# Performance work log

Hardware: AMD Instinct MI355X
Metric: run time of the kernel (lower is better)

The kernel has to match this reference:

```python
import jax, jax.numpy as jnp
import numpy as np

B, S, D = 2, 2048, 1024
H = 16
DK = D // H  # attn_dim // num_heads = 64
DV = D // H  # embed_dim // num_heads = 64
NEG = -1e9


def setup_inputs() -> dict:
    key = jax.random.key(0)
    ks = jax.random.split(key, 6)
    inputs = jax.random.normal(ks[0], (B, S, D), dtype=jnp.float32)
    # mask[b, i, j]: key position i may attend to query position j when i <= j (causal)
    mask = jnp.broadcast_to(jnp.triu(jnp.ones((S, S), dtype=bool))[None], (B, S, S))
    sd = 1.0 / np.sqrt(D)
    WQ = jax.random.normal(ks[1], (D, H, DK), dtype=jnp.float32) * sd
    WK = jax.random.normal(ks[2], (D, H, DK), dtype=jnp.float32) * sd
    WV = jax.random.normal(ks[3], (D, H, DV), dtype=jnp.float32) * sd
    WO = jax.random.normal(ks[4], (D, D), dtype=jnp.float32) * sd
    bO = jnp.zeros((D,), dtype=jnp.float32)
    return {"inputs": inputs, "mask": mask, "WQ": WQ, "WK": WK, "WV": WV, "WO": WO, "bO": bO}


def reference(inputs, mask, WQ, WK, WV, WO, bO):
    scale = 1.0 / jnp.sqrt(jnp.float32(DK))
    q = jnp.einsum('bid,dhk->bihk', inputs, WQ) * scale
    k = jnp.einsum('bid,dhk->bihk', inputs, WK)
    v = jnp.einsum('bid,dhv->bihv', inputs, WV)
    # scores: [b, i, j, h]; softmax over axis=1 (key axis i), as in the original
    scores = jnp.einsum('bihd,bjhd->bijh', q, k)
    scores = jnp.where(mask[..., None], scores, NEG)
    attn = jax.nn.softmax(scores, axis=1)
    x = jnp.einsum('bijh,bihv->bjhv', attn, v)  # output indexed by query j
    x = x.reshape(B, S, D)
    return x @ WO + bO
```

## Files before the change

kernel.cpp:

```cpp
#include <hip/hip_runtime.h>
#include <hip/hip_bf16.h>


typedef __bf16 bf16;
typedef __bf16 bf16x8 __attribute__((ext_vector_type(8)));
typedef __bf16 bf16x4 __attribute__((ext_vector_type(4)));
typedef float  f32x4  __attribute__((ext_vector_type(4)));

constexpr int Sq = 2048;
constexpr int Dm = 1024;
constexpr int Hh = 16;

#define KSCALE 0.18033688011112042f

static __device__ __forceinline__ void gload_lds16(const bf16* g, bf16* l) {
  __builtin_amdgcn_global_load_lds(
      (const __attribute__((address_space(1))) unsigned int*)g,
      (__attribute__((address_space(3))) unsigned int*)l, 16, 0, 0);
}

__global__ __launch_bounds__(256) void cvt_bf16(
    const float* __restrict__ src, bf16* __restrict__ dst, int n) {
  const int i = (blockIdx.x * 256 + threadIdx.x) * 8;
  if (i >= n) return;
  float4 a = *reinterpret_cast<const float4*>(src + i);
  float4 b = *reinterpret_cast<const float4*>(src + i + 4);
  bf16x8 o;
  o[0] = (bf16)a.x; o[1] = (bf16)a.y; o[2] = (bf16)a.z; o[3] = (bf16)a.w;
  o[4] = (bf16)b.x; o[5] = (bf16)b.y; o[6] = (bf16)b.z; o[7] = (bf16)b.w;
  *reinterpret_cast<bf16x8*>(dst + i) = o;
}

__global__ __launch_bounds__(256) void tposeW4(
    const float* __restrict__ WQ, const float* __restrict__ WK,
    const float* __restrict__ WV, const float* __restrict__ WO,
    bf16* __restrict__ out) {
  __shared__ bf16 t[64][65];
  const int z = blockIdx.z;
  const float* in = (z == 0) ? WQ : (z == 1) ? WK : (z == 2) ? WV : WO;
  bf16* op = out + (size_t)z * 1024 * 1024;
  const int r0 = blockIdx.y * 64, c0 = blockIdx.x * 64;
  const int tid = threadIdx.x;
  const int rr = tid >> 3, cc = (tid & 7) * 8;
#pragma unroll
  for (int it = 0; it < 2; ++it) {
    int row = rr + it * 32;
    const float* ip = in + (size_t)(r0 + row) * 1024 + c0 + cc;
    float4 a = *reinterpret_cast<const float4*>(ip);
    float4 b = *reinterpret_cast<const float4*>(ip + 4);
    t[row][cc + 0] = (bf16)a.x; t[row][cc + 1] = (bf16)a.y;
    t[row][cc + 2] = (bf16)a.z; t[row][cc + 3] = (bf16)a.w;
    t[row][cc + 4] = (bf16)b.x; t[row][cc + 5] = (bf16)b.y;
    t[row][cc + 6] = (bf16)b.z; t[row][cc + 7] = (bf16)b.w;
  }
  __syncthreads();
#pragma unroll
  for (int it = 0; it < 2; ++it) {
    int crow = rr + it * 32;
    alignas(16) bf16 o[8];
#pragma unroll
    for (int e = 0; e < 8; ++e) o[e] = t[cc + e][crow];
    *reinterpret_cast<bf16x8*>(op + (size_t)(c0 + crow) * 1024 + r0 + cc) =
        *reinterpret_cast<bf16x8*>(o);
  }
}

template <int EPI, int MT>
__global__ __launch_bounds__(256) void gemm128(
    const bf16* __restrict__ A, const bf16* __restrict__ Bt,
    const int M, const int N, const int K,
    bf16* __restrict__ Katt, bf16* __restrict__ Qatt, bf16* __restrict__ VattT,
    const float* __restrict__ bOf, float* __restrict__ Cout) {
  constexpr int MF = MT / 32;
  __shared__ bf16 As[MT * 64], Bs[8192];
  const int tid = threadIdx.x;
  const int lane = tid & 63;
  const int w = tid >> 6;
  const int wr = w >> 1, wc = w & 1;
  const int g = lane >> 4, c = lane & 15;
  const int m0 = blockIdx.y * MT, n0 = blockIdx.x * 128;
  const int sr = lane >> 3;
  const int scp = ((lane & 7) ^ sr) * 8;

  f32x4 acc[MF][4];
#pragma unroll
  for (int i = 0; i < MF; ++i)
#pragma unroll
    for (int j = 0; j < 4; ++j) acc[i][j] = f32x4{0.f, 0.f, 0.f, 0.f};

  for (int k0 = 0; k0 < K; k0 += 64) {
#pragma unroll
    for (int p = 0; p < MT / 32; ++p) {
      const int rowb = p * 32 + w * 8;
      gload_lds16(A + (size_t)(m0 + rowb + sr) * K + k0 + scp, &As[rowb * 64]);
    }
#pragma unroll
    for (int p = 0; p < 4; ++p) {
      const int rowb = p * 32 + w * 8;
      gload_lds16(Bt + (size_t)(n0 + rowb + sr) * K + k0 + scp, &Bs[rowb * 64]);
    }
    __syncthreads();
#pragma unroll
    for (int kk = 0; kk < 2; ++kk) {
      const int ch = kk * 4 + g;
      bf16x8 af[MF], bfr[4];
#pragma unroll
      for (int mf = 0; mf < MF; ++mf) {
        const int row = wr * (MT / 2) + mf * 16 + c;
        af[mf] = *reinterpret_cast<const bf16x8*>(
            &As[row * 64 + ((ch ^ (row & 7)) << 3)]);
      }
#pragma unroll
      for (int nf = 0; nf < 4; ++nf) {
        const int row = wc * 64 + nf * 16 + c;
        bfr[nf] = *reinterpret_cast<const bf16x8*>(
            &Bs[row * 64 + ((ch ^ (row & 7)) << 3)]);
      }
#pragma unroll
      for (int mf = 0; mf < MF; ++mf)
#pragma unroll
        for (int nf = 0; nf < 4; ++nf)
          acc[mf][nf] = __builtin_amdgcn_mfma_f32_16x16x32_bf16(
              af[mf], bfr[nf], acc[mf][nf], 0, 0, 0);
    }
    __syncthreads();
  }

#pragma unroll
  for (int mf = 0; mf < MF; ++mf)
#pragma unroll
    for (int nf = 0; nf < 4; ++nf) {
      const int n = n0 + wc * 64 + nf * 16 + c;
      const int mb = m0 + wr * (MT / 2) + mf * 16 + g * 4;
      if (EPI == 0 && n >= 2048) {
        bf16x4 pk;
#pragma unroll
        for (int r = 0; r < 4; ++r) pk[r] = (bf16)acc[mf][nf][r];
        const int b = mb >> 11, sb = mb & (Sq - 1);
        const int h = (n >> 6) & 15, dk = n & 63;
        *reinterpret_cast<bf16x4*>(
            &VattT[((size_t)(b * Hh + h) * 64 + dk) * Sq + sb]) = pk;
      } else {
#pragma unroll
        for (int r = 0; r < 4; ++r) {
          const int m = mb + r;
          float v = acc[mf][nf][r];
          if (EPI == 0) {
            const int b = m >> 11, s = m & (Sq - 1);
            const int h = (n >> 6) & 15, dk = n & 63;
            const int bh = b * Hh + h;
            if (n < 1024)
              Katt[((size_t)bh * Sq + s) * 64 + dk] = (bf16)(v * KSCALE);
            else
              Qatt[((size_t)bh * Sq + s) * 64 + dk] = (bf16)v;
          } else {
            Cout[(size_t)m * N + n] = v + bOf[n];
          }
        }
      }
    }
}

__global__ __launch_bounds__(256, 4) void attn_v4(
    const bf16* __restrict__ Q, const bf16* __restrict__ K,
    const bf16* __restrict__ Vt, bf16* __restrict__ X) {
  __shared__ bf16 Kb[2][4096];
  __shared__ bf16 Vb[2][4096];
  __shared__ bf16 Pb[4096];
  const int tid = threadIdx.x, lane = tid & 63, w = tid >> 6;
  const int g = lane >> 4, c = lane & 15;
  const int bx = blockIdx.x;
  const int u = bx >> 5;
  const int bh = bx & 31;
  const int um = (u + 8 * (bh >> 3)) & 31;
  const int qblk = (um < 16) ? um : 47 - um;
  const int b = bh >> 4, h = bh & 15;
  const size_t base = (size_t)bh * Sq * 64;
  const bf16* Kg = K + base;
  const bf16* Vg = Vt + (size_t)bh * 64 * Sq;
  const int trow = tid >> 3, tch = tid & 7;
  bf16* Pw = Pb + w * 16 * 64;

  bf16x8 qf[2];
  {
    const bf16* Qg = Q + base + ((size_t)qblk * 64 + w * 16 + c) * 64;
    qf[0] = *reinterpret_cast<const bf16x8*>(Qg + g * 8);
    qf[1] = *reinterpret_cast<const bf16x8*>(Qg + 32 + g * 8);
  }

#pragma unroll
  for (int pp = 0; pp < 2; ++pp) {
    int row = trow + pp * 32;
    *reinterpret_cast<bf16x8*>(&Kb[0][row * 64 + ((tch ^ (row & 7)) << 3)]) =
        *reinterpret_cast<const bf16x8*>(Kg + (size_t)row * 64 + tch * 8);
    *reinterpret_cast<bf16x8*>(&Vb[0][row * 64 + ((tch ^ (row & 7)) << 3)]) =
        *reinterpret_cast<const bf16x8*>(Vg + (size_t)row * Sq + tch * 8);
  }
  __syncthreads();

  f32x4 acc[4];
  float lpart[4] = {0.f, 0.f, 0.f, 0.f};
#pragma unroll
  for (int vg = 0; vg < 4; ++vg) acc[vg] = f32x4{0.f, 0.f, 0.f, 0.f};

  const int ntiles = qblk + 1;
  for (int t = 0; t < ntiles; ++t) {
    const int cur = t & 1;
    const bf16* Kc = Kb[cur];
    const bf16* Vc = Vb[cur];
    const bool hasnext = (t + 1 < ntiles);

    bf16x8 kr0, kr1, vr0, vr1;
    if (hasnext) {
      const int i1 = (t + 1) * 64;
      kr0 = *reinterpret_cast<const bf16x8*>(Kg + (size_t)(i1 + trow) * 64 + tch * 8);
      kr1 = *reinterpret_cast<const bf16x8*>(Kg + (size_t)(i1 + trow + 32) * 64 + tch * 8);
      vr0 = *reinterpret_cast<const bf16x8*>(Vg + (size_t)trow * Sq + i1 + tch * 8);
      vr1 = *reinterpret_cast<const bf16x8*>(Vg + (size_t)(trow + 32) * Sq + i1 + tch * 8);
    }

    f32x4 sc[4];
#pragma unroll
    for (int kg = 0; kg < 4; ++kg) sc[kg] = f32x4{0.f, 0.f, 0.f, 0.f};
#pragma unroll
    for (int kk = 0; kk < 2; ++kk) {
      const int ch = kk * 4 + g;
#pragma unroll
      for (int kg = 0; kg < 4; ++kg) {
        int row = kg * 16 + c;
        bf16x8 kf = *reinterpret_cast<const bf16x8*>(
            &Kc[row * 64 + ((ch ^ (row & 7)) << 3)]);
        sc[kg] = __builtin_amdgcn_mfma_f32_16x16x32_bf16(qf[kk], kf, sc[kg], 0, 0, 0);
      }
    }

    const bool diag = (t == qblk);
#pragma unroll
    for (int kg = 0; kg < 4; ++kg)
#pragma unroll
      for (int r = 0; r < 4; ++r) {
        float p = __builtin_amdgcn_exp2f(sc[kg][r]);
        if (diag) {
          const int i = kg * 16 + c;
          const int j = w * 16 + g * 4 + r;
          p = (i <= j) ? p : 0.f;
        }
        lpart[r] += p;
        const int prow = g * 4 + r, pcol = kg * 16 + c;
        Pw[prow * 64 + (((pcol >> 3) ^ (prow & 7)) << 3) + (pcol & 7)] = (bf16)p;
      }

#pragma unroll
    for (int ks = 0; ks < 2; ++ks) {
      const int ch = ks * 4 + g;
      bf16x8 pf = *reinterpret_cast<const bf16x8*>(
          &Pw[c * 64 + ((ch ^ (c & 7)) << 3)]);
#pragma unroll
      for (int vg = 0; vg < 4; ++vg) {
        int dv = vg * 16 + c;
        bf16x8 vf = *reinterpret_cast<const bf16x8*>(
            &Vc[dv * 64 + ((ch ^ (dv & 7)) << 3)]);
        acc[vg] = __builtin_amdgcn_mfma_f32_16x16x32_bf16(pf, vf, acc[vg], 0, 0, 0);
      }
    }

    if (hasnext) {
      bf16* Kn = Kb[cur ^ 1];
      bf16* Vn = Vb[cur ^ 1];
      const int row0 = trow, row1 = trow + 32;
      *reinterpret_cast<bf16x8*>(&Kn[row0 * 64 + ((tch ^ (row0 & 7)) << 3)]) = kr0;
      *reinterpret_cast<bf16x8*>(&Kn[row1 * 64 + ((tch ^ (row1 & 7)) << 3)]) = kr1;
      *reinterpret_cast<bf16x8*>(&Vn[row0 * 64 + ((tch ^ (row0 & 7)) << 3)]) = vr0;
      *reinterpret_cast<bf16x8*>(&Vn[row1 * 64 + ((tch ^ (row1 & 7)) << 3)]) = vr1;
    }
    __syncthreads();
  }

  float linv[4];
#pragma unroll
  for (int r = 0; r < 4; ++r) {
    float l = lpart[r];
    l += __shfl_xor(l, 1);
    l += __shfl_xor(l, 2);
    l += __shfl_xor(l, 4);
    l += __shfl_xor(l, 8);
    linv[r] = 1.f / l;
  }
#pragma unroll
  for (int vg = 0; vg < 4; ++vg)
#pragma unroll
    for (int r = 0; r < 4; ++r) {
      const int j = qblk * 64 + w * 16 + g * 4 + r;
      const int dv = vg * 16 + c;
      X[((size_t)b * Sq + j) * Dm + h * 64 + dv] = (bf16)(acc[vg][r] * linv[r]);
    }
}

extern "C" void kernel_launch(void* const* d_in, const int* in_sizes, int n_in,
                              void* d_out, int out_size, void* d_ws, size_t ws_size,
                              hipStream_t stream) {
  const float* inputs = (const float*)d_in[0];
  const float* WQ = (const float*)d_in[2];
  const float* WK = (const float*)d_in[3];
  const float* WV = (const float*)d_in[4];
  const float* WO = (const float*)d_in[5];
  const float* bO = (const float*)d_in[6];
  float* out = (float*)d_out;

  bf16* Xin   = (bf16*)d_ws;
  bf16* Wt    = Xin + 4096 * 1024;
  bf16* Katt  = Wt + 4 * 1024 * 1024;
  bf16* Qatt  = Katt + (1 << 22);
  bf16* VattT = Qatt + (1 << 22);
  bf16* X     = Xin;

  cvt_bf16<<<2048, 256, 0, stream>>>(inputs, Xin, 4096 * 1024);

  tposeW4<<<dim3(16, 16, 4), 256, 0, stream>>>(WQ, WK, WV, WO, Wt);

  gemm128<0, 128><<<dim3(24, 32), 256, 0, stream>>>(
      Xin, Wt, 4096, 3072, 1024, Katt, Qatt, VattT, nullptr, nullptr);

  attn_v4<<<dim3(1024), 256, 0, stream>>>(Qatt, Katt, VattT, X);

  gemm128<1, 64><<<dim3(8, 64), 256, 0, stream>>>(
      X, Wt + 3 * 1024 * 1024, 4096, 1024, 1024,
      nullptr, nullptr, nullptr, bO, out);
}
```

Before: 108.2 us.

## Load K/V fragments directly from global in attention and merge prep kernels

The attention kernel drops the double-buffered LDS staging of K and V tiles along with the per-tile __syncthreads. Each wave now loads its MFMA operand fragments straight from global memory, relying on L2/L1 to serve the reuse across the four waves of a block. Separately, the bf16 input conversion and the weight transpose are merged into one launch to save a kernel launch. The risk is more global traffic and exposed load latency, since there is no longer an explicit prefetch of the next tile.

```diff
diff --git a/kernel.cpp b/kernel.cpp
--- a/kernel.cpp
+++ b/kernel.cpp
@@ -19,28 +19,30 @@
       (__attribute__((address_space(3))) unsigned int*)l, 16, 0, 0);
 }
 
-__global__ __launch_bounds__(256) void cvt_bf16(
-    const float* __restrict__ src, bf16* __restrict__ dst, int n) {
-  const int i = (blockIdx.x * 256 + threadIdx.x) * 8;
-  if (i >= n) return;
-  float4 a = *reinterpret_cast<const float4*>(src + i);
-  float4 b = *reinterpret_cast<const float4*>(src + i + 4);
-  bf16x8 o;
-  o[0] = (bf16)a.x; o[1] = (bf16)a.y; o[2] = (bf16)a.z; o[3] = (bf16)a.w;
-  o[4] = (bf16)b.x; o[5] = (bf16)b.y; o[6] = (bf16)b.z; o[7] = (bf16)b.w;
-  *reinterpret_cast<bf16x8*>(dst + i) = o;
-}
-
-__global__ __launch_bounds__(256) void tposeW4(
+__global__ __launch_bounds__(256) void prep(
+    const float* __restrict__ inputs,
     const float* __restrict__ WQ, const float* __restrict__ WK,
     const float* __restrict__ WV, const float* __restrict__ WO,
-    bf16* __restrict__ out) {
+    bf16* __restrict__ Xin, bf16* __restrict__ Wt) {
   __shared__ bf16 t[64][65];
-  const int z = blockIdx.z;
+  const int bx = blockIdx.x;
+  const int tid = threadIdx.x;
+  if (bx < 2048) {
+    const int i = (bx * 256 + tid) * 8;
+    float4 a = *reinterpret_cast<const float4*>(inputs + i);
+    float4 b = *reinterpret_cast<const float4*>(inputs + i + 4);
+    bf16x8 o;
+    o[0] = (bf16)a.x; o[1] = (bf16)a.y; o[2] = (bf16)a.z; o[3] = (bf16)a.w;
+    o[4] = (bf16)b.x; o[5] = (bf16)b.y; o[6] = (bf16)b.z; o[7] = (bf16)b.w;
+    *reinterpret_cast<bf16x8*>(Xin + i) = o;
+    return;
+  }
+  const int rr0 = bx - 2048;
+  const int z = rr0 >> 8;
+  const int tt = rr0 & 255;
+  const int r0 = (tt >> 4) * 64, c0 = (tt & 15) * 64;
   const float* in = (z == 0) ? WQ : (z == 1) ? WK : (z == 2) ? WV : WO;
-  bf16* op = out + (size_t)z * 1024 * 1024;
-  const int r0 = blockIdx.y * 64, c0 = blockIdx.x * 64;
-  const int tid = threadIdx.x;
+  bf16* op = Wt + (size_t)z * 1024 * 1024;
   const int rr = tid >> 3, cc = (tid & 7) * 8;
 #pragma unroll
   for (int it = 0; it < 2; ++it) {
@@ -161,11 +163,9 @@
     }
 }
 
-__global__ __launch_bounds__(256, 4) void attn_v4(
+__global__ __launch_bounds__(256, 4) void attn_v5(
     const bf16* __restrict__ Q, const bf16* __restrict__ K,
     const bf16* __restrict__ Vt, bf16* __restrict__ X) {
-  __shared__ bf16 Kb[2][4096];
-  __shared__ bf16 Vb[2][4096];
   __shared__ bf16 Pb[4096];
   const int tid = threadIdx.x, lane = tid & 63, w = tid >> 6;
   const int g = lane >> 4, c = lane & 15;
@@ -178,8 +178,7 @@
   const size_t base = (size_t)bh * Sq * 64;
   const bf16* Kg = K + base;
   const bf16* Vg = Vt + (size_t)bh * 64 * Sq;
-  const int trow = tid >> 3, tch = tid & 7;
-  bf16* Pw = Pb + w * 16 * 64;
+  bf16* Pw = Pb + w * 1024;
 
   bf16x8 qf[2];
   {
@@ -188,16 +187,6 @@
     qf[1] = *reinterpret_cast<const bf16x8*>(Qg + 32 + g * 8);
   }
 
-#pragma unroll
-  for (int pp = 0; pp < 2; ++pp) {
-    int row = trow + pp * 32;
-    *reinterpret_cast<bf16x8*>(&Kb[0][row * 64 + ((tch ^ (row & 7)) << 3)]) =
-        *reinterpret_cast<const bf16x8*>(Kg + (size_t)row * 64 + tch * 8);
-    *reinterpret_cast<bf16x8*>(&Vb[0][row * 64 + ((tch ^ (row & 7)) << 3)]) =
-        *reinterpret_cast<const bf16x8*>(Vg + (size_t)row * Sq + tch * 8);
-  }
-  __syncthreads();
-
   f32x4 acc[4];
   float lpart[4] = {0.f, 0.f, 0.f, 0.f};
 #pragma unroll
@@ -205,34 +194,32 @@
 
   const int ntiles = qblk + 1;
   for (int t = 0; t < ntiles; ++t) {
-    const int cur = t & 1;
-    const bf16* Kc = Kb[cur];
-    const bf16* Vc = Vb[cur];
-    const bool hasnext = (t + 1 < ntiles);
-
-    bf16x8 kr0, kr1, vr0, vr1;
-    if (hasnext) {
-      const int i1 = (t + 1) * 64;
-      kr0 = *reinterpret_cast<const bf16x8*>(Kg + (size_t)(i1 + trow) * 64 + tch * 8);
-      kr1 = *reinterpret_cast<const bf16x8*>(Kg + (size_t)(i1 + trow + 32) * 64 + tch * 8);
-      vr0 = *reinterpret_cast<const bf16x8*>(Vg + (size_t)trow * Sq + i1 + tch * 8);
-      vr1 = *reinterpret_cast<const bf16x8*>(Vg + (size_t)(trow + 32) * Sq + i1 + tch * 8);
-    }
+    const bf16* Kt = Kg + (size_t)t * 64 * 64;
+    bf16x8 kf[2][4];
+#pragma unroll
+    for (int kk = 0; kk < 2; ++kk)
+#pragma unroll
+      for (int kg = 0; kg < 4; ++kg)
+        kf[kk][kg] = *reinterpret_cast<const bf16x8*>(
+            Kt + (kg * 16 + c) * 64 + kk * 32 + g * 8);
 
     f32x4 sc[4];
 #pragma unroll
     for (int kg = 0; kg < 4; ++kg) sc[kg] = f32x4{0.f, 0.f, 0.f, 0.f};
 #pragma unroll
-    for (int kk = 0; kk < 2; ++kk) {
-      const int ch = kk * 4 + g;
-#pragma unroll
-      for (int kg = 0; kg < 4; ++kg) {
-        int row = kg * 16 + c;
-        bf16x8 kf = *reinterpret_cast<const bf16x8*>(
-            &Kc[row * 64 + ((ch ^ (row & 7)) << 3)]);
-        sc[kg] = __builtin_amdgcn_mfma_f32_16x16x32_bf16(qf[kk], kf, sc[kg], 0, 0, 0);
-      }
-    }
+    for (int kk = 0; kk < 2; ++kk)
+#pragma unroll
+      for (int kg = 0; kg < 4; ++kg)
+        sc[kg] = __builtin_amdgcn_mfma_f32_16x16x32_bf16(
+            qf[kk], kf[kk][kg], sc[kg], 0, 0, 0);
+
+    bf16x8 vf[2][4];
+#pragma unroll
+    for (int ks = 0; ks < 2; ++ks)
+#pragma unroll
+      for (int vg = 0; vg < 4; ++vg)
+        vf[ks][vg] = *reinterpret_cast<const bf16x8*>(
+            Vg + (size_t)(vg * 16 + c) * Sq + t * 64 + ks * 32 + g * 8);
 
     const bool diag = (t == qblk);
 #pragma unroll
@@ -256,24 +243,10 @@
       bf16x8 pf = *reinterpret_cast<const bf16x8*>(
           &Pw[c * 64 + ((ch ^ (c & 7)) << 3)]);
 #pragma unroll
-      for (int vg = 0; vg < 4; ++vg) {
-        int dv = vg * 16 + c;
-        bf16x8 vf = *reinterpret_cast<const bf16x8*>(
-            &Vc[dv * 64 + ((ch ^ (dv & 7)) << 3)]);
-        acc[vg] = __builtin_amdgcn_mfma_f32_16x16x32_bf16(pf, vf, acc[vg], 0, 0, 0);
-      }
-    }
-
-    if (hasnext) {
-      bf16* Kn = Kb[cur ^ 1];
-      bf16* Vn = Vb[cur ^ 1];
-      const int row0 = trow, row1 = trow + 32;
-      *reinterpret_cast<bf16x8*>(&Kn[row0 * 64 + ((tch ^ (row0 & 7)) << 3)]) = kr0;
-      *reinterpret_cast<bf16x8*>(&Kn[row1 * 64 + ((tch ^ (row1 & 7)) << 3)]) = kr1;
-      *reinterpret_cast<bf16x8*>(&Vn[row0 * 64 + ((tch ^ (row0 & 7)) << 3)]) = vr0;
-      *reinterpret_cast<bf16x8*>(&Vn[row1 * 64 + ((tch ^ (row1 & 7)) << 3)]) = vr1;
-    }
-    __syncthreads();
+      for (int vg = 0; vg < 4; ++vg)
+        acc[vg] = __builtin_amdgcn_mfma_f32_16x16x32_bf16(
+            pf, vf[ks][vg], acc[vg], 0, 0, 0);
+    }
   }
 
   float linv[4];
@@ -314,14 +287,12 @@
   bf16* VattT = Qatt + (1 << 22);
   bf16* X     = Xin;
 
-  cvt_bf16<<<2048, 256, 0, stream>>>(inputs, Xin, 4096 * 1024);
-
-  tposeW4<<<dim3(16, 16, 4), 256, 0, stream>>>(WQ, WK, WV, WO, Wt);
+  prep<<<3072, 256, 0, stream>>>(inputs, WQ, WK, WV, WO, Xin, Wt);
 
   gemm128<0, 128><<<dim3(24, 32), 256, 0, stream>>>(
       Xin, Wt, 4096, 3072, 1024, Katt, Qatt, VattT, nullptr, nullptr);
 
-  attn_v4<<<dim3(1024), 256, 0, stream>>>(Qatt, Katt, VattT, X);
+  attn_v5<<<dim3(1024), 256, 0, stream>>>(Qatt, Katt, VattT, X);
 
   gemm128<1, 64><<<dim3(8, 64), 256, 0, stream>>>(
       X, Wt + 3 * 1024 * 1024, 4096, 1024, 1024,
```

Result: slower. 183.6 us (+69.6%).

## Process two query blocks per attention workgroup and merge prep kernels

Applied to the files above, without the earlier changes.

The attention kernel now handles 128 query rows per workgroup (two 64-row sub-blocks) so that each K/V tile loaded into LDS feeds twice as many MFMAs. The grid halves to 512 blocks and the causal load-balancing remap is adjusted. On the final tile only the second sub-block is active. The launch bound drops to 2 waves per SIMD, and register pressure and P buffer size grow. Separately, the input cast and weight transpose kernels are fused into one launch to save a kernel launch.

```diff
diff --git a/kernel.cpp b/kernel.cpp
--- a/kernel.cpp
+++ b/kernel.cpp
@@ -19,28 +19,30 @@
       (__attribute__((address_space(3))) unsigned int*)l, 16, 0, 0);
 }
 
-__global__ __launch_bounds__(256) void cvt_bf16(
-    const float* __restrict__ src, bf16* __restrict__ dst, int n) {
-  const int i = (blockIdx.x * 256 + threadIdx.x) * 8;
-  if (i >= n) return;
-  float4 a = *reinterpret_cast<const float4*>(src + i);
-  float4 b = *reinterpret_cast<const float4*>(src + i + 4);
-  bf16x8 o;
-  o[0] = (bf16)a.x; o[1] = (bf16)a.y; o[2] = (bf16)a.z; o[3] = (bf16)a.w;
-  o[4] = (bf16)b.x; o[5] = (bf16)b.y; o[6] = (bf16)b.z; o[7] = (bf16)b.w;
-  *reinterpret_cast<bf16x8*>(dst + i) = o;
-}
-
-__global__ __launch_bounds__(256) void tposeW4(
+__global__ __launch_bounds__(256) void prep(
+    const float* __restrict__ inputs,
     const float* __restrict__ WQ, const float* __restrict__ WK,
     const float* __restrict__ WV, const float* __restrict__ WO,
-    bf16* __restrict__ out) {
+    bf16* __restrict__ Xin, bf16* __restrict__ Wt) {
   __shared__ bf16 t[64][65];
-  const int z = blockIdx.z;
+  const int bx = blockIdx.x;
+  const int tid = threadIdx.x;
+  if (bx < 2048) {
+    const int i = (bx * 256 + tid) * 8;
+    float4 a = *reinterpret_cast<const float4*>(inputs + i);
+    float4 b = *reinterpret_cast<const float4*>(inputs + i + 4);
+    bf16x8 o;
+    o[0] = (bf16)a.x; o[1] = (bf16)a.y; o[2] = (bf16)a.z; o[3] = (bf16)a.w;
+    o[4] = (bf16)b.x; o[5] = (bf16)b.y; o[6] = (bf16)b.z; o[7] = (bf16)b.w;
+    *reinterpret_cast<bf16x8*>(Xin + i) = o;
+    return;
+  }
+  const int rr0 = bx - 2048;
+  const int z = rr0 >> 8;
+  const int tt = rr0 & 255;
+  const int r0 = (tt >> 4) * 64, c0 = (tt & 15) * 64;
   const float* in = (z == 0) ? WQ : (z == 1) ? WK : (z == 2) ? WV : WO;
-  bf16* op = out + (size_t)z * 1024 * 1024;
-  const int r0 = blockIdx.y * 64, c0 = blockIdx.x * 64;
-  const int tid = threadIdx.x;
+  bf16* op = Wt + (size_t)z * 1024 * 1024;
   const int rr = tid >> 3, cc = (tid & 7) * 8;
 #pragma unroll
   for (int it = 0; it < 2; ++it) {
@@ -161,31 +163,31 @@
     }
 }
 
-__global__ __launch_bounds__(256, 4) void attn_v4(
+__global__ __launch_bounds__(256, 2) void attn_v7(
     const bf16* __restrict__ Q, const bf16* __restrict__ K,
     const bf16* __restrict__ Vt, bf16* __restrict__ X) {
   __shared__ bf16 Kb[2][4096];
   __shared__ bf16 Vb[2][4096];
-  __shared__ bf16 Pb[4096];
+  __shared__ bf16 Pb[8192];
   const int tid = threadIdx.x, lane = tid & 63, w = tid >> 6;
   const int g = lane >> 4, c = lane & 15;
   const int bx = blockIdx.x;
   const int u = bx >> 5;
   const int bh = bx & 31;
-  const int um = (u + 8 * (bh >> 3)) & 31;
-  const int qblk = (um < 16) ? um : 47 - um;
+  const int um = (u + 4 * (bh >> 3)) & 15;
+  const int qblk = (um < 8) ? um : 23 - um;
   const int b = bh >> 4, h = bh & 15;
   const size_t base = (size_t)bh * Sq * 64;
   const bf16* Kg = K + base;
   const bf16* Vg = Vt + (size_t)bh * 64 * Sq;
   const int trow = tid >> 3, tch = tid & 7;
-  bf16* Pw = Pb + w * 16 * 64;
-
-  bf16x8 qf[2];
-  {
-    const bf16* Qg = Q + base + ((size_t)qblk * 64 + w * 16 + c) * 64;
-    qf[0] = *reinterpret_cast<const bf16x8*>(Qg + g * 8);
-    qf[1] = *reinterpret_cast<const bf16x8*>(Qg + 32 + g * 8);
+
+  bf16x8 qf[2][2];
+#pragma unroll
+  for (int z = 0; z < 2; ++z) {
+    const bf16* Qg = Q + base + ((size_t)qblk * 128 + z * 64 + w * 16 + c) * 64;
+    qf[z][0] = *reinterpret_cast<const bf16x8*>(Qg + g * 8);
+    qf[z][1] = *reinterpret_cast<const bf16x8*>(Qg + 32 + g * 8);
   }
 
 #pragma unroll
@@ -198,17 +200,23 @@
   }
   __syncthreads();
 
-  f32x4 acc[4];
-  float lpart[4] = {0.f, 0.f, 0.f, 0.f};
-#pragma unroll
-  for (int vg = 0; vg < 4; ++vg) acc[vg] = f32x4{0.f, 0.f, 0.f, 0.f};
-
-  const int ntiles = qblk + 1;
+  f32x4 acc[2][4];
+  float lpart[2][4];
+#pragma unroll
+  for (int z = 0; z < 2; ++z)
+#pragma unroll
+    for (int r = 0; r < 4; ++r) {
+      lpart[z][r] = 0.f;
+      acc[z][r] = f32x4{0.f, 0.f, 0.f, 0.f};
+    }
+
+  const int ntiles = 2 * qblk + 2;
   for (int t = 0; t < ntiles; ++t) {
     const int cur = t & 1;
     const bf16* Kc = Kb[cur];
     const bf16* Vc = Vb[cur];
     const bool hasnext = (t + 1 < ntiles);
+    const bool act0 = (t != ntiles - 1);
 
     bf16x8 kr0, kr1, vr0, vr1;
     if (hasnext) {
@@ -219,48 +227,71 @@
       vr1 = *reinterpret_cast<const bf16x8*>(Vg + (size_t)(trow + 32) * Sq + i1 + tch * 8);
     }
 
-    f32x4 sc[4];
-#pragma unroll
-    for (int kg = 0; kg < 4; ++kg) sc[kg] = f32x4{0.f, 0.f, 0.f, 0.f};
+    f32x4 sc[2][4];
+#pragma unroll
+    for (int z = 0; z < 2; ++z)
+#pragma unroll
+      for (int kg = 0; kg < 4; ++kg) sc[z][kg] = f32x4{0.f, 0.f, 0.f, 0.f};
 #pragma unroll
     for (int kk = 0; kk < 2; ++kk) {
       const int ch = kk * 4 + g;
+      bf16x8 kf[4];
 #pragma unroll
       for (int kg = 0; kg < 4; ++kg) {
         int row = kg * 16 + c;
-        bf16x8 kf = *reinterpret_cast<const bf16x8*>(
+        kf[kg] = *reinterpret_cast<const bf16x8*>(
             &Kc[row * 64 + ((ch ^ (row & 7)) << 3)]);
-        sc[kg] = __builtin_amdgcn_mfma_f32_16x16x32_bf16(qf[kk], kf, sc[kg], 0, 0, 0);
-      }
-    }
-
-    const bool diag = (t == qblk);
-#pragma unroll
-    for (int kg = 0; kg < 4; ++kg)
-#pragma unroll
-      for (int r = 0; r < 4; ++r) {
-        float p = __builtin_amdgcn_exp2f(sc[kg][r]);
-        if (diag) {
-          const int i = kg * 16 + c;
-          const int j = w * 16 + g * 4 + r;
-          p = (i <= j) ? p : 0.f;
+      }
+#pragma unroll
+      for (int kg = 0; kg < 4; ++kg) {
+        sc[1][kg] = __builtin_amdgcn_mfma_f32_16x16x32_bf16(
+            qf[1][kk], kf[kg], sc[1][kg], 0, 0, 0);
+        if (act0)
+          sc[0][kg] = __builtin_amdgcn_mfma_f32_16x16x32_bf16(
+              qf[0][kk], kf[kg], sc[0][kg], 0, 0, 0);
+      }
+    }
+
+#pragma unroll
+    for (int z = 0; z < 2; ++z) {
+      if (z == 0 && !act0) continue;
+      const bool diag = (z == 0) ? (t == ntiles - 2) : (t == ntiles - 1);
+      bf16* Pz = Pb + (size_t)(w * 2 + z) * 1024;
+#pragma unroll
+      for (int kg = 0; kg < 4; ++kg)
+#pragma unroll
+        for (int r = 0; r < 4; ++r) {
+          float p = __builtin_amdgcn_exp2f(sc[z][kg][r]);
+          if (diag) {
+            const int i = t * 64 + kg * 16 + c;
+            const int j = qblk * 128 + z * 64 + w * 16 + g * 4 + r;
+            p = (i <= j) ? p : 0.f;
+          }
+          lpart[z][r] += p;
+          const int prow = g * 4 + r, pcol = kg * 16 + c;
+          Pz[prow * 64 + (((pcol >> 3) ^ (prow & 7)) << 3) + (pcol & 7)] = (bf16)p;
         }
-        lpart[r] += p;
-        const int prow = g * 4 + r, pcol = kg * 16 + c;
-        Pw[prow * 64 + (((pcol >> 3) ^ (prow & 7)) << 3) + (pcol & 7)] = (bf16)p;
-      }
+    }
 
 #pragma unroll
     for (int ks = 0; ks < 2; ++ks) {
       const int ch = ks * 4 + g;
-      bf16x8 pf = *reinterpret_cast<const bf16x8*>(
-          &Pw[c * 64 + ((ch ^ (c & 7)) << 3)]);
+      bf16x8 pf1 = *reinterpret_cast<const bf16x8*>(
+          &Pb[(size_t)(w * 2 + 1) * 1024 + c * 64 + ((ch ^ (c & 7)) << 3)]);
+      bf16x8 pf0;
+      if (act0)
+        pf0 = *reinterpret_cast<const bf16x8*>(
+            &Pb[(size_t)(w * 2 + 0) * 1024 + c * 64 + ((ch ^ (c & 7)) << 3)]);
 #pragma unroll
       for (int vg = 0; vg < 4; ++vg) {
         int dv = vg * 16 + c;
         bf16x8 vf = *reinterpret_cast<const bf16x8*>(
             &Vc[dv * 64 + ((ch ^ (dv & 7)) << 3)]);
-        acc[vg] = __builtin_amdgcn_mfma_f32_16x16x32_bf16(pf, vf, acc[vg], 0, 0, 0);
+        acc[1][vg] = __builtin_amdgcn_mfma_f32_16x16x32_bf16(
+            pf1, vf, acc[1][vg], 0, 0, 0);
+        if (act0)
+          acc[0][vg] = __builtin_amdgcn_mfma_f32_16x16x32_bf16(
+              pf0, vf, acc[0][vg], 0, 0, 0);
       }
     }
 
@@ -276,24 +307,27 @@
     __syncthreads();
   }
 
-  float linv[4];
-#pragma unroll
-  for (int r = 0; r < 4; ++r) {
-    float l = lpart[r];
-    l += __shfl_xor(l, 1);
-    l += __shfl_xor(l, 2);
-    l += __shfl_xor(l, 4);
-    l += __shfl_xor(l, 8);
-    linv[r] = 1.f / l;
-  }
-#pragma unroll
-  for (int vg = 0; vg < 4; ++vg)
+#pragma unroll
+  for (int z = 0; z < 2; ++z) {
+    float linv[4];
 #pragma unroll
     for (int r = 0; r < 4; ++r) {
-      const int j = qblk * 64 + w * 16 + g * 4 + r;
-      const int dv = vg * 16 + c;
-      X[((size_t)b * Sq + j) * Dm + h * 64 + dv] = (bf16)(acc[vg][r] * linv[r]);
-    }
+      float l = lpart[z][r];
+      l += __shfl_xor(l, 1);
+      l += __shfl_xor(l, 2);
+      l += __shfl_xor(l, 4);
+      l += __shfl_xor(l, 8);
+      linv[r] = 1.f / l;
+    }
+#pragma unroll
+    for (int vg = 0; vg < 4; ++vg)
+#pragma unroll
+      for (int r = 0; r < 4; ++r) {
+        const int j = qblk * 128 + z * 64 + w * 16 + g * 4 + r;
+        const int dv = vg * 16 + c;
+        X[((size_t)b * Sq + j) * Dm + h * 64 + dv] = (bf16)(acc[z][vg][r] * linv[r]);
+      }
+  }
 }
 
 extern "C" void kernel_launch(void* const* d_in, const int* in_sizes, int n_in,
@@ -314,14 +348,12 @@
   bf16* VattT = Qatt + (1 << 22);
   bf16* X     = Xin;
 
-  cvt_bf16<<<2048, 256, 0, stream>>>(inputs, Xin, 4096 * 1024);
-
-  tposeW4<<<dim3(16, 16, 4), 256, 0, stream>>>(WQ, WK, WV, WO, Wt);
+  prep<<<3072, 256, 0, stream>>>(inputs, WQ, WK, WV, WO, Xin, Wt);
 
   gemm128<0, 128><<<dim3(24, 32), 256, 0, stream>>>(
       Xin, Wt, 4096, 3072, 1024, Katt, Qatt, VattT, nullptr, nullptr);
 
-  attn_v4<<<dim3(1024), 256, 0, stream>>>(Qatt, Katt, VattT, X);
+  attn_v7<<<dim3(512), 256, 0, stream>>>(Qatt, Katt, VattT, X);
 
   gemm128<1, 64><<<dim3(8, 64), 256, 0, stream>>>(
       X, Wt + 3 * 1024 * 1024, 4096, 1024, 1024,
```

Result: faster. 103.7 us (-4.1%).

## Pair causal query blocks per attention workgroup and merge prep kernels

Applied to the files above, without the earlier changes.

The attention kernel now has each workgroup process two query blocks (p and 31-p), so every block does an equal amount of causal work. The grid halves to 512 blocks and the occupancy hint drops from 4 to 2. Separately, the bf16 conversion and weight transpose kernels are merged into a single launch to save one kernel launch. The risk is less parallelism: 512 blocks on 256 CUs gives no spare blocks to hide latency, and the two query blocks run one after the other within a block.

```diff
diff --git a/kernel.cpp b/kernel.cpp
--- a/kernel.cpp
+++ b/kernel.cpp
@@ -19,28 +19,30 @@
       (__attribute__((address_space(3))) unsigned int*)l, 16, 0, 0);
 }
 
-__global__ __launch_bounds__(256) void cvt_bf16(
-    const float* __restrict__ src, bf16* __restrict__ dst, int n) {
-  const int i = (blockIdx.x * 256 + threadIdx.x) * 8;
-  if (i >= n) return;
-  float4 a = *reinterpret_cast<const float4*>(src + i);
-  float4 b = *reinterpret_cast<const float4*>(src + i + 4);
-  bf16x8 o;
-  o[0] = (bf16)a.x; o[1] = (bf16)a.y; o[2] = (bf16)a.z; o[3] = (bf16)a.w;
-  o[4] = (bf16)b.x; o[5] = (bf16)b.y; o[6] = (bf16)b.z; o[7] = (bf16)b.w;
-  *reinterpret_cast<bf16x8*>(dst + i) = o;
-}
-
-__global__ __launch_bounds__(256) void tposeW4(
+__global__ __launch_bounds__(256) void prep(
+    const float* __restrict__ inputs,
     const float* __restrict__ WQ, const float* __restrict__ WK,
     const float* __restrict__ WV, const float* __restrict__ WO,
-    bf16* __restrict__ out) {
+    bf16* __restrict__ Xin, bf16* __restrict__ Wt) {
   __shared__ bf16 t[64][65];
-  const int z = blockIdx.z;
+  const int bx = blockIdx.x;
+  const int tid = threadIdx.x;
+  if (bx < 2048) {
+    const int i = (bx * 256 + tid) * 8;
+    float4 a = *reinterpret_cast<const float4*>(inputs + i);
+    float4 b = *reinterpret_cast<const float4*>(inputs + i + 4);
+    bf16x8 o;
+    o[0] = (bf16)a.x; o[1] = (bf16)a.y; o[2] = (bf16)a.z; o[3] = (bf16)a.w;
+    o[4] = (bf16)b.x; o[5] = (bf16)b.y; o[6] = (bf16)b.z; o[7] = (bf16)b.w;
+    *reinterpret_cast<bf16x8*>(Xin + i) = o;
+    return;
+  }
+  const int rr0 = bx - 2048;
+  const int z = rr0 >> 8;
+  const int tt = rr0 & 255;
+  const int r0 = (tt >> 4) * 64, c0 = (tt & 15) * 64;
   const float* in = (z == 0) ? WQ : (z == 1) ? WK : (z == 2) ? WV : WO;
-  bf16* op = out + (size_t)z * 1024 * 1024;
-  const int r0 = blockIdx.y * 64, c0 = blockIdx.x * 64;
-  const int tid = threadIdx.x;
+  bf16* op = Wt + (size_t)z * 1024 * 1024;
   const int rr = tid >> 3, cc = (tid & 7) * 8;
 #pragma unroll
   for (int it = 0; it < 2; ++it) {
@@ -161,7 +163,7 @@
     }
 }
 
-__global__ __launch_bounds__(256, 4) void attn_v4(
+__global__ __launch_bounds__(256, 2) void attn_v9(
     const bf16* __restrict__ Q, const bf16* __restrict__ K,
     const bf16* __restrict__ Vt, bf16* __restrict__ X) {
   __shared__ bf16 Kb[2][4096];
@@ -170,130 +172,135 @@
   const int tid = threadIdx.x, lane = tid & 63, w = tid >> 6;
   const int g = lane >> 4, c = lane & 15;
   const int bx = blockIdx.x;
-  const int u = bx >> 5;
+  const int p = bx >> 5;
   const int bh = bx & 31;
-  const int um = (u + 8 * (bh >> 3)) & 31;
-  const int qblk = (um < 16) ? um : 47 - um;
   const int b = bh >> 4, h = bh & 15;
   const size_t base = (size_t)bh * Sq * 64;
   const bf16* Kg = K + base;
   const bf16* Vg = Vt + (size_t)bh * 64 * Sq;
   const int trow = tid >> 3, tch = tid & 7;
-  bf16* Pw = Pb + w * 16 * 64;
-
-  bf16x8 qf[2];
-  {
-    const bf16* Qg = Q + base + ((size_t)qblk * 64 + w * 16 + c) * 64;
-    qf[0] = *reinterpret_cast<const bf16x8*>(Qg + g * 8);
-    qf[1] = *reinterpret_cast<const bf16x8*>(Qg + 32 + g * 8);
-  }
-
-#pragma unroll
-  for (int pp = 0; pp < 2; ++pp) {
-    int row = trow + pp * 32;
-    *reinterpret_cast<bf16x8*>(&Kb[0][row * 64 + ((tch ^ (row & 7)) << 3)]) =
-        *reinterpret_cast<const bf16x8*>(Kg + (size_t)row * 64 + tch * 8);
-    *reinterpret_cast<bf16x8*>(&Vb[0][row * 64 + ((tch ^ (row & 7)) << 3)]) =
-        *reinterpret_cast<const bf16x8*>(Vg + (size_t)row * Sq + tch * 8);
-  }
-  __syncthreads();
-
-  f32x4 acc[4];
-  float lpart[4] = {0.f, 0.f, 0.f, 0.f};
-#pragma unroll
-  for (int vg = 0; vg < 4; ++vg) acc[vg] = f32x4{0.f, 0.f, 0.f, 0.f};
-
-  const int ntiles = qblk + 1;
-  for (int t = 0; t < ntiles; ++t) {
-    const int cur = t & 1;
-    const bf16* Kc = Kb[cur];
-    const bf16* Vc = Vb[cur];
-    const bool hasnext = (t + 1 < ntiles);
-
-    bf16x8 kr0, kr1, vr0, vr1;
-    if (hasnext) {
-      const int i1 = (t + 1) * 64;
-      kr0 = *reinterpret_cast<const bf16x8*>(Kg + (size_t)(i1 + trow) * 64 + tch * 8);
-      kr1 = *reinterpret_cast<const bf16x8*>(Kg + (size_t)(i1 + trow + 32) * 64 + tch * 8);
-      vr0 = *reinterpret_cast<const bf16x8*>(Vg + (size_t)trow * Sq + i1 + tch * 8);
-      vr1 = *reinterpret_cast<const bf16x8*>(Vg + (size_t)(trow + 32) * Sq + i1 + tch * 8);
-    }
-
-    f32x4 sc[4];
-#pragma unroll
-    for (int kg = 0; kg < 4; ++kg) sc[kg] = f32x4{0.f, 0.f, 0.f, 0.f};
-#pragma unroll
-    for (int kk = 0; kk < 2; ++kk) {
-      const int ch = kk * 4 + g;
-#pragma unroll
-      for (int kg = 0; kg < 4; ++kg) {
-        int row = kg * 16 + c;
-        bf16x8 kf = *reinterpret_cast<const bf16x8*>(
-            &Kc[row * 64 + ((ch ^ (row & 7)) << 3)]);
-        sc[kg] = __builtin_amdgcn_mfma_f32_16x16x32_bf16(qf[kk], kf, sc[kg], 0, 0, 0);
-      }
-    }
-
-    const bool diag = (t == qblk);
-#pragma unroll
-    for (int kg = 0; kg < 4; ++kg)
+  bf16* Pw = Pb + w * 1024;
+
+#pragma unroll
+  for (int z = 0; z < 2; ++z) {
+    const int qblk = z ? (31 - p) : p;
+
+    bf16x8 qf[2];
+    {
+      const bf16* Qg = Q + base + ((size_t)qblk * 64 + w * 16 + c) * 64;
+      qf[0] = *reinterpret_cast<const bf16x8*>(Qg + g * 8);
+      qf[1] = *reinterpret_cast<const bf16x8*>(Qg + 32 + g * 8);
+    }
+
+#pragma unroll
+    for (int pp = 0; pp < 2; ++pp) {
+      int row = trow + pp * 32;
+      *reinterpret_cast<bf16x8*>(&Kb[0][row * 64 + ((tch ^ (row & 7)) << 3)]) =
+          *reinterpret_cast<const bf16x8*>(Kg + (size_t)row * 64 + tch * 8);
+      *reinterpret_cast<bf16x8*>(&Vb[0][row * 64 + ((tch ^ (row & 7)) << 3)]) =
+          *reinterpret_cast<const bf16x8*>(Vg + (size_t)row * Sq + tch * 8);
+    }
+    __syncthreads();
+
+    f32x4 acc[4];
+    float lpart[4] = {0.f, 0.f, 0.f, 0.f};
+#pragma unroll
+    for (int vg = 0; vg < 4; ++vg) acc[vg] = f32x4{0.f, 0.f, 0.f, 0.f};
+
+    const int ntiles = qblk + 1;
+    for (int t = 0; t < ntiles; ++t) {
+      const int cur = t & 1;
+      const bf16* Kc = Kb[cur];
+      const bf16* Vc = Vb[cur];
+      const bool hasnext = (t + 1 < ntiles);
+
+      bf16x8 kr0, kr1, vr0, vr1;
+      if (hasnext) {
+        const int i1 = (t + 1) * 64;
+        kr0 = *reinterpret_cast<const bf16x8*>(Kg + (size_t)(i1 + trow) * 64 + tch * 8);
+        kr1 = *reinterpret_cast<const bf16x8*>(Kg + (size_t)(i1 + trow + 32) * 64 + tch * 8);
+        vr0 = *reinterpret_cast<const bf16x8*>(Vg + (size_t)trow * Sq + i1 + tch * 8);
+        vr1 = *reinterpret_cast<const bf16x8*>(Vg + (size_t)(trow + 32) * Sq + i1 + tch * 8);
+      }
+
+      f32x4 sc[4];
+#pragma unroll
+      for (int kg = 0; kg < 4; ++kg) sc[kg] = f32x4{0.f, 0.f, 0.f, 0.f};
+#pragma unroll
+      for (int kk = 0; kk < 2; ++kk) {
+        const int ch = kk * 4 + g;
+#pragma unroll
+        for (int kg = 0; kg < 4; ++kg) {
+          int row = kg * 16 + c;
+          bf16x8 kf = *reinterpret_cast<const bf16x8*>(
+              &Kc[row * 64 + ((ch ^ (row & 7)) << 3)]);
+          sc[kg] = __builtin_amdgcn_mfma_f32_16x16x32_bf16(
+              qf[kk], kf, sc[kg], 0, 0, 0);
+        }
+      }
+
+      const bool diag = (t == qblk);
+#pragma unroll
+      for (int kg = 0; kg < 4; ++kg)
+#pragma unroll
+        for (int r = 0; r < 4; ++r) {
+          float pv = __builtin_amdgcn_exp2f(sc[kg][r]);
+          if (diag) {
+            const int i = kg * 16 + c;
+            const int j = w * 16 + g * 4 + r;
+            pv = (i <= j) ? pv : 0.f;
+          }
+          lpart[r] += pv;
+          const int prow = g * 4 + r, pcol = kg * 16 + c;
+          Pw[prow * 64 + (((pcol >> 3) ^ (prow & 7)) << 3) + (pcol & 7)] = (bf16)pv;
+        }
+
+#pragma unroll
+      for (int ks = 0; ks < 2; ++ks) {
+        const int ch = ks * 4 + g;
+        bf16x8 pf = *reinterpret_cast<const bf16x8*>(
+            &Pw[c * 64 + ((ch ^ (c & 7)) << 3)]);
+#pragma unroll
+        for (int vg = 0; vg < 4; ++vg) {
+          int dv = vg * 16 + c;
+          bf16x8 vf = *reinterpret_cast<const bf16x8*>(
+              &Vc[dv * 64 + ((ch ^ (dv & 7)) << 3)]);
+          acc[vg] = __builtin_amdgcn_mfma_f32_16x16x32_bf16(
+              pf, vf, acc[vg], 0, 0, 0);
+        }
+      }
+
+      if (hasnext) {
+        bf16* Kn = Kb[cur ^ 1];
+        bf16* Vn = Vb[cur ^ 1];
+        const int row0 = trow, row1 = trow + 32;
+        *reinterpret_cast<bf16x8*>(&Kn[row0 * 64 + ((tch ^ (row0 & 7)) << 3)]) = kr0;
+        *reinterpret_cast<bf16x8*>(&Kn[row1 * 64 + ((tch ^ (row1 & 7)) << 3)]) = kr1;
+        *reinterpret_cast<bf16x8*>(&Vn[row0 * 64 + ((tch ^ (row0 & 7)) << 3)]) = vr0;
+        *reinterpret_cast<bf16x8*>(&Vn[row1 * 64 + ((tch ^ (row1 & 7)) << 3)]) = vr1;
+      }
+      __syncthreads();
+    }
+
+    float linv[4];
+#pragma unroll
+    for (int r = 0; r < 4; ++r) {
+      float l = lpart[r];
+      l += __shfl_xor(l, 1);
+      l += __shfl_xor(l, 2);
+      l += __shfl_xor(l, 4);
+      l += __shfl_xor(l, 8);
+      linv[r] = 1.f / l;
+    }
+#pragma unroll
+    for (int vg = 0; vg < 4; ++vg)
 #pragma unroll
       for (int r = 0; r < 4; ++r) {
-        float p = __builtin_amdgcn_exp2f(sc[kg][r]);
-        if (diag) {
-          const int i = kg * 16 + c;
-          const int j = w * 16 + g * 4 + r;
-          p = (i <= j) ? p : 0.f;
-        }
-        lpart[r] += p;
-        const int prow = g * 4 + r, pcol = kg * 16 + c;
-        Pw[prow * 64 + (((pcol >> 3) ^ (prow & 7)) << 3) + (pcol & 7)] = (bf16)p;
-      }
-
-#pragma unroll
-    for (int ks = 0; ks < 2; ++ks) {
-      const int ch = ks * 4 + g;
-      bf16x8 pf = *reinterpret_cast<const bf16x8*>(
-          &Pw[c * 64 + ((ch ^ (c & 7)) << 3)]);
-#pragma unroll
-      for (int vg = 0; vg < 4; ++vg) {
-        int dv = vg * 16 + c;
-        bf16x8 vf = *reinterpret_cast<const bf16x8*>(
-            &Vc[dv * 64 + ((ch ^ (dv & 7)) << 3)]);
-        acc[vg] = __builtin_amdgcn_mfma_f32_16x16x32_bf16(pf, vf, acc[vg], 0, 0, 0);
-      }
-    }
-
-    if (hasnext) {
-      bf16* Kn = Kb[cur ^ 1];
-      bf16* Vn = Vb[cur ^ 1];
-      const int row0 = trow, row1 = trow + 32;
-      *reinterpret_cast<bf16x8*>(&Kn[row0 * 64 + ((tch ^ (row0 & 7)) << 3)]) = kr0;
-      *reinterpret_cast<bf16x8*>(&Kn[row1 * 64 + ((tch ^ (row1 & 7)) << 3)]) = kr1;
-      *reinterpret_cast<bf16x8*>(&Vn[row0 * 64 + ((tch ^ (row0 & 7)) << 3)]) = vr0;
-      *reinterpret_cast<bf16x8*>(&Vn[row1 * 64 + ((tch ^ (row1 & 7)) << 3)]) = vr1;
-    }
-    __syncthreads();
-  }
-
-  float linv[4];
-#pragma unroll
-  for (int r = 0; r < 4; ++r) {
-    float l = lpart[r];
-    l += __shfl_xor(l, 1);
-    l += __shfl_xor(l, 2);
-    l += __shfl_xor(l, 4);
-    l += __shfl_xor(l, 8);
-    linv[r] = 1.f / l;
-  }
-#pragma unroll
-  for (int vg = 0; vg < 4; ++vg)
-#pragma unroll
-    for (int r = 0; r < 4; ++r) {
-      const int j = qblk * 64 + w * 16 + g * 4 + r;
-      const int dv = vg * 16 + c;
-      X[((size_t)b * Sq + j) * Dm + h * 64 + dv] = (bf16)(acc[vg][r] * linv[r]);
-    }
+        const int j = qblk * 64 + w * 16 + g * 4 + r;
+        const int dv = vg * 16 + c;
+        X[((size_t)b * Sq + j) * Dm + h * 64 + dv] = (bf16)(acc[vg][r] * linv[r]);
+      }
+  }
 }
 
 extern "C" void kernel_launch(void* const* d_in, const int* in_sizes, int n_in,
@@ -314,14 +321,12 @@
   bf16* VattT = Qatt + (1 << 22);
   bf16* X     = Xin;
 
-  cvt_bf16<<<2048, 256, 0, stream>>>(inputs, Xin, 4096 * 1024);
-
-  tposeW4<<<dim3(16, 16, 4), 256, 0, stream>>>(WQ, WK, WV, WO, Wt);
+  prep<<<3072, 256, 0, stream>>>(inputs, WQ, WK, WV, WO, Xin, Wt);
 
   gemm128<0, 128><<<dim3(24, 32), 256, 0, stream>>>(
       Xin, Wt, 4096, 3072, 1024, Katt, Qatt, VattT, nullptr, nullptr);
 
-  attn_v4<<<dim3(1024), 256, 0, stream>>>(Qatt, Katt, VattT, X);
+  attn_v9<<<dim3(512), 256, 0, stream>>>(Qatt, Katt, VattT, X);
 
   gemm128<1, 64><<<dim3(8, 64), 256, 0, stream>>>(
       X, Wt + 3 * 1024 * 1024, 4096, 1024, 1024,
```

After: 104.5 us. 1.04x faster.
